# Kernel tuning notes

Hardware: AMD Instinct MI355X
Metric: run time of the kernel (lower is better)

Reference implementation:

```python
import jax, jax.numpy as jnp
import numpy as np

B, T, C, H = 4, 4096, 1024, 64

def setup_inputs() -> dict:
    key = jax.random.key(0)
    kx, kq, kk, kv = jax.random.split(key, 4)
    x = jax.random.normal(kx, (B, T, C), dtype=jnp.float32)
    scale = 1.0 / np.sqrt(C)
    Wq = jax.random.normal(kq, (C, H), dtype=jnp.float32) * scale
    Wk = jax.random.normal(kk, (C, H), dtype=jnp.float32) * scale
    Wv = jax.random.normal(kv, (C, H), dtype=jnp.float32) * scale
    return {"x": x, "Wq": Wq, "Wk": Wk, "Wv": Wv}

def reference(x, Wq, Wk, Wv):
    Bsz, Tlen, _ = x.shape
    head_size = Wq.shape[1]
    q = x @ Wq  # [B,T,H]
    k = x @ Wk
    v = x @ Wv
    # scores [B,T,T], scaled by sqrt(head_size)
    scores = jnp.einsum('bqh,bkh->bqk', q, k) / jnp.sqrt(jnp.float32(head_size))
    causal = jnp.tril(jnp.ones((Tlen, Tlen), dtype=bool))
    scores = jnp.where(causal, scores, -jnp.inf)
    weights = jax.nn.softmax(scores, axis=-1)
    # dropout p=0.0 -> identity
    return jnp.einsum('bqk,bkh->bqh', weights, v)
```

## Files before the change

kernel.cpp:

```cpp
#include <hip/hip_runtime.h>
#include <hip/hip_bf16.h>

typedef __attribute__((ext_vector_type(8))) short short8;
typedef __attribute__((ext_vector_type(4))) float f32x4;

#define MFMA16(a, b, c) __builtin_amdgcn_mfma_f32_16x16x32_bf16((a), (b), (c), 0, 0, 0)

typedef const __attribute__((address_space(1))) unsigned int* gas_t;
typedef __attribute__((address_space(3))) unsigned int* las_t;
#define GLDS16(g, l) __builtin_amdgcn_global_load_lds((gas_t)(g), (las_t)(l), 16, 0, 0)

__device__ inline unsigned short f2bf(float f) {
    union { float f; unsigned int u; } v;
    v.f = f;
    unsigned int u = v.u;
    return (unsigned short)((u + 0x7fffu + ((u >> 16) & 1u)) >> 16);
}

__device__ inline float bf2f(unsigned short u) {
    union { unsigned int u; float f; } v;
    v.u = ((unsigned int)u) << 16;
    return v.f;
}

__device__ inline size_t WF(int n, int c) {
    return ((((size_t)(n >> 4)) * 32 + (c >> 5)) * 64 + ((c >> 3) & 3) * 16 + (n & 15)) * 8 + (c & 7);
}
__device__ inline size_t QKF(int q, int h) {
    return ((((size_t)(q >> 4)) * 2 + (h >> 5)) * 64 + ((h >> 3) & 3) * 16 + (q & 15)) * 8 + (h & 7);
}
__device__ inline size_t VF(int h, int t) {
    return ((((size_t)(h >> 4)) * 128 + (t >> 5)) * 64 + ((t >> 3) & 3) * 16 + (h & 15)) * 8 + (t & 7);
}

__global__ __launch_bounds__(256) void prep_w(const float* __restrict__ Wq,
                                              const float* __restrict__ Wk,
                                              const float* __restrict__ Wv,
                                              unsigned short* __restrict__ Wt) {
    int idx = blockIdx.x * 256 + threadIdx.x;
    if (idx >= 192 * 1024) return;
    int n = idx >> 10;
    int c = idx & 1023;
    const float* W = (n < 64) ? Wq : ((n < 128) ? Wk : Wv);
    float v = W[c * 64 + (n & 63)];
    if (n < 64) v *= 0.125f;
    Wt[WF(n, c)] = f2bf(v);
}

__global__ __launch_bounds__(256, 4) void projt(const float* __restrict__ x,
                                                const unsigned short* __restrict__ Wt,
                                                unsigned short* __restrict__ Qs,
                                                unsigned short* __restrict__ Ks,
                                                unsigned short* __restrict__ Vt) {
    __shared__ __align__(16) float xbuf[2][16 * 128];

    const int tid = threadIdx.x;
    const int w = tid >> 6;
    const int lane = tid & 63;
    const int lr = lane & 15;
    const int lg = lane >> 4;
    const int t0 = blockIdx.x * 16;

    f32x4 acc[3];
#pragma unroll
    for (int i = 0; i < 3; i++) acc[i] = (f32x4){0.f, 0.f, 0.f, 0.f};

#define STAGE_X(buf, c0)                                                       \
    {                                                                          \
        _Pragma("unroll")                                                      \
        for (int p = 0; p < 2; p++) {                                          \
            int row = w * 4 + p * 2 + (lane >> 5);                             \
            int chunk = (lane & 31) ^ (row & 7);                               \
            const float* src = x + (size_t)(t0 + row) * 1024 + (c0) + chunk * 4;\
            float* dst = &xbuf[buf][(w * 4 + p * 2) * 128];  \
            GLDS16(src, dst);                                                  \
        }                                                                      \
    }

    STAGE_X(0, 0);
    __syncthreads();

    int cur = 0;
    for (int t = 0; t < 8; ++t) {
        if (t < 7) STAGE_X(cur ^ 1, (t + 1) * 128);

        const char* xb = (const char*)&xbuf[cur][0];
#pragma unroll
        for (int h = 0; h < 4; h++) {
            short8 bfr[3];
#pragma unroll
            for (int nt = 0; nt < 3; nt++)
                bfr[nt] = *(const short8*)(Wt +
                    (((size_t)(w * 3 + nt) * 32 + (t * 4 + h)) * 64 + lane) * 8);
            int cb = h * 8 + lg * 2;
            float4 a0 = *(const float4*)(xb + lr * 512 + ((cb) ^ (lr & 7)) * 16);
            float4 a1 = *(const float4*)(xb + lr * 512 + ((cb + 1) ^ (lr & 7)) * 16);
            short8 a;
            a[0] = (short)f2bf(a0.x); a[1] = (short)f2bf(a0.y);
            a[2] = (short)f2bf(a0.z); a[3] = (short)f2bf(a0.w);
            a[4] = (short)f2bf(a1.x); a[5] = (short)f2bf(a1.y);
            a[6] = (short)f2bf(a1.z); a[7] = (short)f2bf(a1.w);
#pragma unroll
            for (int nt = 0; nt < 3; nt++) acc[nt] = MFMA16(a, bfr[nt], acc[nt]);
        }
        __syncthreads();
        cur ^= 1;
    }

    const int nbase = w * 48;
#pragma unroll
    for (int nt = 0; nt < 3; nt++) {
#pragma unroll
        for (int r = 0; r < 4; r++) {
            int n = nbase + nt * 16 + lr;
            int tq = t0 + lg * 4 + r;
            int b = tq >> 12;
            int qq = tq & 4095;
            unsigned short val = f2bf(acc[nt][r]);
            if (n < 64) {
                Qs[(size_t)b * 262144 + QKF(qq, n)] = val;
            } else if (n < 128) {
                Ks[(size_t)b * 262144 + QKF(qq, n - 64)] = val;
            } else {
                Vt[(size_t)b * 262144 + VF(n - 128, qq)] = val;
            }
        }
    }
}

#define SROW 72

template <int NS>
__global__ __launch_bounds__(64) void attn(const unsigned short* __restrict__ Qs,
                                           const unsigned short* __restrict__ Ks,
                                           const unsigned short* __restrict__ Vt,
                                           float* __restrict__ out,
                                           unsigned short* __restrict__ accP,
                                           float* __restrict__ mP,
                                           float* __restrict__ lP) {
    __shared__ unsigned short pl[32 * SROW];

    const int ntasks = 512 * NS;
    int raw = ntasks - 1 - blockIdx.x;
    int qt_g = raw / NS;
    int c = raw - qt_g * NS;
    int qt = qt_g >> 2;
    int b = qt_g & 3;
    int q0 = qt * 32;

    int lane = threadIdx.x;
    int lr = lane & 15;
    int lg = lane >> 4;

    const unsigned short* Qb = Qs + (size_t)b * 262144;
    const unsigned short* Kb = Ks + (size_t)b * 262144;
    const unsigned short* Vb = Vt + (size_t)b * 262144;

    short8 qf[2][2];
#pragma unroll
    for (int qs = 0; qs < 2; qs++)
#pragma unroll
        for (int kh = 0; kh < 2; kh++)
            qf[qs][kh] = *(const short8*)(Qb +
                (((size_t)((q0 >> 4) + qs) * 2 + kh) * 64 + lane) * 8);

    f32x4 acc[4][2];
#pragma unroll
    for (int i = 0; i < 4; i++)
#pragma unroll
        for (int qs = 0; qs < 2; qs++) acc[i][qs] = (f32x4){0.f, 0.f, 0.f, 0.f};
    float m[2] = {-1e30f, -1e30f};
    float l[2] = {0.f, 0.f};

    int nt = (q0 + 95) >> 6;
    int tb = (c * nt) / NS;
    int te = ((c + 1) * nt) / NS;

    short8 kf[4][2];
    if (tb < te) {
#pragma unroll
        for (int t = 0; t < 4; t++)
#pragma unroll
            for (int half = 0; half < 2; half++)
                kf[t][half] = *(const short8*)(Kb +
                    (((size_t)((tb * 64) >> 4) + t) * 2 + half) * 512 + lane * 8);
    }

    for (int t64 = tb; t64 < te; ++t64) {
        int kv0 = t64 * 64;

        f32x4 s[4][2];
#pragma unroll
        for (int t = 0; t < 4; t++)
#pragma unroll
            for (int qs = 0; qs < 2; qs++) {
                f32x4 z = (f32x4){0.f, 0.f, 0.f, 0.f};
                z = MFMA16(kf[t][0], qf[qs][0], z);
                z = MFMA16(kf[t][1], qf[qs][1], z);
                s[t][qs] = z;
            }

        short8 vf[4][2];
#pragma unroll
        for (int ht = 0; ht < 4; ht++)
#pragma unroll
            for (int half = 0; half < 2; half++)
                vf[ht][half] = *(const short8*)(Vb +
                    (((size_t)ht * 128 + (kv0 >> 5) + half) * 64 + lane) * 8);

        if (t64 + 1 < te) {
            int kvn = (t64 + 1) * 64;
#pragma unroll
            for (int t = 0; t < 4; t++)
#pragma unroll
                for (int half = 0; half < 2; half++)
                    kf[t][half] = *(const short8*)(Kb +
                        (((size_t)(kvn >> 4) + t) * 2 + half) * 512 + lane * 8);
        }

        if (kv0 + 63 > q0) {
#pragma unroll
            for (int t = 0; t < 4; t++)
#pragma unroll
                for (int qs = 0; qs < 2; qs++)
#pragma unroll
                    for (int r = 0; r < 4; r++) {
                        int kv = kv0 + t * 16 + lg * 4 + r;
                        if (kv > q0 + qs * 16 + lr) s[t][qs][r] = -1e30f;
                    }
        }

        float pmax[2] = {-1e30f, -1e30f};
#pragma unroll
        for (int t = 0; t < 4; t++)
#pragma unroll
            for (int qs = 0; qs < 2; qs++)
#pragma unroll
                for (int r = 0; r < 4; r++) pmax[qs] = fmaxf(pmax[qs], s[t][qs][r]);

        int ok = (pmax[0] <= m[0] + 8.0f) && (pmax[1] <= m[1] + 8.0f);
        if (!__all(ok)) {
            float alpha[2];
#pragma unroll
            for (int qs = 0; qs < 2; qs++) {
                float mx = pmax[qs];
                mx = fmaxf(mx, __shfl_xor(mx, 16));
                mx = fmaxf(mx, __shfl_xor(mx, 32));
                float mn = fmaxf(m[qs], mx);
                alpha[qs] = __expf(m[qs] - mn);
                m[qs] = mn;
                l[qs] *= alpha[qs];
            }
            float ar[2][4];
#pragma unroll
            for (int qs = 0; qs < 2; qs++)
#pragma unroll
                for (int r = 0; r < 4; r++) ar[qs][r] = __shfl(alpha[qs], lg * 4 + r);
#pragma unroll
            for (int ht = 0; ht < 4; ht++)
#pragma unroll
                for (int qs = 0; qs < 2; qs++)
#pragma unroll
                    for (int r = 0; r < 4; r++) acc[ht][qs][r] *= ar[qs][r];
        }

#pragma unroll
        for (int t = 0; t < 4; t++)
#pragma unroll
            for (int qs = 0; qs < 2; qs++)
#pragma unroll
                for (int r = 0; r < 4; r++) {
                    float e = __expf(s[t][qs][r] - m[qs]);
                    s[t][qs][r] = e;
                    l[qs] += e;
                }

#pragma unroll
        for (int qs = 0; qs < 2; qs++)
#pragma unroll
            for (int t = 0; t < 4; t++) {
                uint2 uu;
                uu.x = (unsigned)f2bf(s[t][qs][0]) | ((unsigned)f2bf(s[t][qs][1]) << 16);
                uu.y = (unsigned)f2bf(s[t][qs][2]) | ((unsigned)f2bf(s[t][qs][3]) << 16);
                *(uint2*)&pl[(qs * 16 + lr) * SROW + t * 16 + lg * 4] = uu;
            }
        asm volatile("s_waitcnt lgkmcnt(0)" ::: "memory");
        __builtin_amdgcn_sched_barrier(0);
        short8 pa[2][2];
#pragma unroll
        for (int qs = 0; qs < 2; qs++)
#pragma unroll
            for (int half = 0; half < 2; half++)
                pa[qs][half] = *(const short8*)&pl[(qs * 16 + lr) * SROW +
                                                   half * 32 + lg * 8];

#pragma unroll
        for (int ht = 0; ht < 4; ht++)
#pragma unroll
            for (int qs = 0; qs < 2; qs++) {
                acc[ht][qs] = MFMA16(pa[qs][0], vf[ht][0], acc[ht][qs]);
                acc[ht][qs] = MFMA16(pa[qs][1], vf[ht][1], acc[ht][qs]);
            }
    }

    float lt[2];
#pragma unroll
    for (int qs = 0; qs < 2; qs++) {
        float v = l[qs];
        v += __shfl_xor(v, 16);
        v += __shfl_xor(v, 32);
        lt[qs] = v;
    }

    if (NS == 1) {
        float rl[2][4];
#pragma unroll
        for (int qs = 0; qs < 2; qs++)
#pragma unroll
            for (int r = 0; r < 4; r++) rl[qs][r] = 1.0f / __shfl(lt[qs], lg * 4 + r);
#pragma unroll
        for (int ht = 0; ht < 4; ht++)
#pragma unroll
            for (int qs = 0; qs < 2; qs++)
#pragma unroll
                for (int r = 0; r < 4; r++) {
                    size_t o = ((size_t)b * 4096 + q0 + qs * 16 + lg * 4 + r) * 64 +
                               ht * 16 + lr;
                    out[o] = acc[ht][qs][r] * rl[qs][r];
                }
    } else {
        int tidx = qt_g * NS + c;
        unsigned short* ap = accP + (size_t)tidx * 2048;
#pragma unroll
        for (int ht = 0; ht < 4; ht++)
#pragma unroll
            for (int qs = 0; qs < 2; qs++)
#pragma unroll
                for (int r = 0; r < 4; r++)
                    ap[(qs * 16 + lg * 4 + r) * 64 + ht * 16 + lr] =
                        f2bf(acc[ht][qs][r]);
        if (lane < 16) {
#pragma unroll
            for (int qs = 0; qs < 2; qs++) {
                mP[tidx * 32 + qs * 16 + lane] = m[qs];
                lP[tidx * 32 + qs * 16 + lane] = lt[qs];
            }
        }
    }
}

template <int NS>
__global__ __launch_bounds__(256) void combine(const unsigned short* __restrict__ accP,
                                               const float* __restrict__ mP,
                                               const float* __restrict__ lP,
                                               float* __restrict__ out) {
    int g = blockIdx.x * 256 + threadIdx.x;
    int h = g & 63;
    int row = g >> 6;
    int b = row >> 12;
    int t = row & 4095;
    int qt = t >> 5;
    int qr = t & 31;
    int qt_g = qt * 4 + b;

    float mc[NS];
    float M = -1e30f;
#pragma unroll
    for (int c = 0; c < NS; c++) {
        mc[c] = mP[(qt_g * NS + c) * 32 + qr];
        M = fmaxf(M, mc[c]);
    }
    float num = 0.f, den = 0.f;
#pragma unroll
    for (int c = 0; c < NS; c++) {
        float wgt = __expf(mc[c] - M);
        den += wgt * lP[(qt_g * NS + c) * 32 + qr];
        num += wgt * bf2f(accP[(size_t)(qt_g * NS + c) * 2048 + qr * 64 + h]);
    }
    out[g] = num / den;
}

extern "C" void kernel_launch(void* const* d_in, const int* in_sizes, int n_in,
                              void* d_out, int out_size, void* d_ws, size_t ws_size,
                              hipStream_t stream) {
    const float* x  = (const float*)d_in[0];
    const float* Wq = (const float*)d_in[1];
    const float* Wk = (const float*)d_in[2];
    const float* Wv = (const float*)d_in[3];
    float* out = (float*)d_out;

    char* ws = (char*)d_ws;
    unsigned short* Qs = (unsigned short*)(ws);
    unsigned short* Ks = (unsigned short*)(ws + (2u << 20));
    unsigned short* Vt = (unsigned short*)(ws + (4u << 20));
    unsigned short* Wt = (unsigned short*)(ws + (6u << 20));
    unsigned short* accP = (unsigned short*)(ws + (8u << 20));
    float* mP = (float*)(ws + (24u << 20));
    float* lP = (float*)(ws + (24u << 20) + (512u << 10));

    prep_w<<<768, 256, 0, stream>>>(Wq, Wk, Wv, Wt);
    projt<<<1024, 256, 0, stream>>>(x, Wt, Qs, Ks, Vt);

    if (ws_size >= (25u << 20)) {
        attn<8><<<4096, 64, 0, stream>>>(Qs, Ks, Vt, out, accP, mP, lP);
        combine<8><<<4096, 256, 0, stream>>>(accP, mP, lP, out);
    } else {
        attn<1><<<512, 64, 0, stream>>>(Qs, Ks, Vt, out, accP, mP, lP);
    }
}
```

Measured before the change: 71.38 us.

## Stage full x row tile into LDS once and batch weight loads per chunk

The projection kernel now loads the whole 16x1024 fp32 slice of x into shared memory (64 KB) in a single async pass with an XOR swizzle, replacing the double-buffered 128-column pipeline and its per-iteration barriers. All weight fragments for each 128-column chunk are loaded up front so the matrix ops wait less on global memory. The larger shared-memory footprint lowers the occupancy hint from 4 to 2 blocks per CU, and the loads of x can no longer overlap with compute inside a block.

```diff
diff --git a/kernel.cpp b/kernel.cpp
--- a/kernel.cpp
+++ b/kernel.cpp
@@ -47,12 +47,12 @@
     Wt[WF(n, c)] = f2bf(v);
 }
 
-__global__ __launch_bounds__(256, 4) void projt(const float* __restrict__ x,
+__global__ __launch_bounds__(256, 2) void projt(const float* __restrict__ x,
                                                 const unsigned short* __restrict__ Wt,
                                                 unsigned short* __restrict__ Qs,
                                                 unsigned short* __restrict__ Ks,
                                                 unsigned short* __restrict__ Vt) {
-    __shared__ __align__(16) float xbuf[2][16 * 128];
+    __shared__ __align__(16) float xbuf[16 * 1024];
 
     const int tid = threadIdx.x;
     const int w = tid >> 6;
@@ -61,50 +61,49 @@
     const int lg = lane >> 4;
     const int t0 = blockIdx.x * 16;
 
+#pragma unroll
+    for (int rr = 0; rr < 4; rr++) {
+        int r = w * 4 + rr;
+#pragma unroll
+        for (int q = 0; q < 4; q++) {
+            int gc = q * 64 + (lane >> 4) * 16 + ((lane & 15) ^ r);
+            const float* src = x + (size_t)(t0 + r) * 1024 + gc * 4;
+            float* dst = &xbuf[r * 1024 + q * 256];
+            GLDS16(src, dst);
+        }
+    }
+    __syncthreads();
+
     f32x4 acc[3];
 #pragma unroll
     for (int i = 0; i < 3; i++) acc[i] = (f32x4){0.f, 0.f, 0.f, 0.f};
 
-#define STAGE_X(buf, c0)                                                       \
-    {                                                                          \
-        _Pragma("unroll")                                                      \
-        for (int p = 0; p < 2; p++) {                                          \
-            int row = w * 4 + p * 2 + (lane >> 5);                             \
-            int chunk = (lane & 31) ^ (row & 7);                               \
-            const float* src = x + (size_t)(t0 + row) * 1024 + (c0) + chunk * 4;\
-            float* dst = &xbuf[buf][(w * 4 + p * 2) * 128];  \
-            GLDS16(src, dst);                                                  \
-        }                                                                      \
-    }
-
-    STAGE_X(0, 0);
-    __syncthreads();
-
-    int cur = 0;
     for (int t = 0; t < 8; ++t) {
-        if (t < 7) STAGE_X(cur ^ 1, (t + 1) * 128);
-
-        const char* xb = (const char*)&xbuf[cur][0];
+        const int ch0 = t * 32;
+
+        short8 bfr[4][3];
+#pragma unroll
+        for (int h = 0; h < 4; h++)
+#pragma unroll
+            for (int nt = 0; nt < 3; nt++)
+                bfr[h][nt] = *(const short8*)(Wt +
+                    (((size_t)(w * 3 + nt) * 32 + (t * 4 + h)) * 64 + lane) * 8);
+
 #pragma unroll
         for (int h = 0; h < 4; h++) {
-            short8 bfr[3];
-#pragma unroll
-            for (int nt = 0; nt < 3; nt++)
-                bfr[nt] = *(const short8*)(Wt +
-                    (((size_t)(w * 3 + nt) * 32 + (t * 4 + h)) * 64 + lane) * 8);
-            int cb = h * 8 + lg * 2;
-            float4 a0 = *(const float4*)(xb + lr * 512 + ((cb) ^ (lr & 7)) * 16);
-            float4 a1 = *(const float4*)(xb + lr * 512 + ((cb + 1) ^ (lr & 7)) * 16);
+            int cb = ch0 + h * 8 + lg * 2;
+            int l0 = (cb & ~15) | ((cb & 15) ^ lr);
+            int l1 = ((cb + 1) & ~15) | (((cb + 1) & 15) ^ lr);
+            float4 a0 = *(const float4*)&xbuf[lr * 1024 + l0 * 4];
+            float4 a1 = *(const float4*)&xbuf[lr * 1024 + l1 * 4];
             short8 a;
             a[0] = (short)f2bf(a0.x); a[1] = (short)f2bf(a0.y);
             a[2] = (short)f2bf(a0.z); a[3] = (short)f2bf(a0.w);
             a[4] = (short)f2bf(a1.x); a[5] = (short)f2bf(a1.y);
             a[6] = (short)f2bf(a1.z); a[7] = (short)f2bf(a1.w);
 #pragma unroll
-            for (int nt = 0; nt < 3; nt++) acc[nt] = MFMA16(a, bfr[nt], acc[nt]);
-        }
-        __syncthreads();
-        cur ^= 1;
+            for (int nt = 0; nt < 3; nt++) acc[nt] = MFMA16(a, bfr[h][nt], acc[nt]);
+        }
     }
 
     const int nbase = w * 48;
```

Result: no change. 70.35 us, median of 2 (-1.4%).
